# Kernel tuning notes

Measured on AMD Instinct MI355X. Metric: run time of the kernel, lower is better.

## Reference

```python
import jax, jax.numpy as jnp
import numpy as np

INPUT_SIZE = 4
HIDDEN = 100
OUTPUT = 1
SEQ_LEN = 65536


def setup_inputs() -> dict:
    key = jax.random.key(0)
    ks = jax.random.split(key, 7)
    s = 0.1  # small init scale, mimics torch's uniform(-1/sqrt(H), 1/sqrt(H))
    return {
        "input_seq": jax.random.normal(ks[0], (SEQ_LEN, INPUT_SIZE), dtype=jnp.float32),
        "W_ih": jax.random.normal(ks[1], (4 * HIDDEN, INPUT_SIZE), dtype=jnp.float32) * s,
        "W_hh": jax.random.normal(ks[2], (4 * HIDDEN, HIDDEN), dtype=jnp.float32) * s,
        "b_ih": jax.random.normal(ks[3], (4 * HIDDEN,), dtype=jnp.float32) * s,
        "b_hh": jax.random.normal(ks[4], (4 * HIDDEN,), dtype=jnp.float32) * s,
        "W_lin": jax.random.normal(ks[5], (OUTPUT, HIDDEN), dtype=jnp.float32) * s,
        "b_lin": jax.random.normal(ks[6], (OUTPUT,), dtype=jnp.float32) * s,
    }


def reference(input_seq, W_ih, W_hh, b_ih, b_hh, W_lin, b_lin):
    # Precompute the input contribution to all gates in one GEMM: [S, 4H]
    x_gates = input_seq @ W_ih.T + (b_ih + b_hh)

    def step(carry, xg):
        h, c = carry  # each [H]
        gates = xg + h @ W_hh.T  # [4H]
        # torch gate order: i, f, g, o
        i = jax.nn.sigmoid(gates[:HIDDEN])
        f = jax.nn.sigmoid(gates[HIDDEN:2 * HIDDEN])
        g = jnp.tanh(gates[2 * HIDDEN:3 * HIDDEN])
        o = jax.nn.sigmoid(gates[3 * HIDDEN:])
        c_new = f * c + i * g
        h_new = o * jnp.tanh(c_new)
        return (h_new, c_new), None

    h0 = jnp.zeros((HIDDEN,), dtype=input_seq.dtype)
    c0 = jnp.zeros((HIDDEN,), dtype=input_seq.dtype)
    (h_last, _), _ = jax.lax.scan(step, (h0, c0), x_gates)

    # predictions[-1] == linear applied to the last hidden state; shape [OUTPUT]
    return h_last @ W_lin.T + b_lin
```

## Files before the change

### kernel.cpp

```cpp
#include <hip/hip_runtime.h>

#define HIDDEN  100
#define SEQLEN  65536
#define XTILE   256
#define NT      256

typedef float    f32x4 __attribute__((ext_vector_type(4)));
typedef _Float16 h16x2 __attribute__((ext_vector_type(2)));

#define DPP_XOR1 0xB1
#define DPP_XOR2 0x4E

#if defined(__has_builtin) && __has_builtin(__builtin_amdgcn_rcpf)
#define RCPF(x) __builtin_amdgcn_rcpf(x)
#else
#define RCPF(x) (1.0f / (x))
#endif

#define QSWAP(v, ctrl) __int_as_float(__builtin_amdgcn_mov_dpp(__float_as_int(v), (ctrl), 0xf, 0xf, true))

static __device__ __forceinline__ h16x2 as_h2(unsigned u) {
    union { unsigned u; h16x2 h; } cv; cv.u = u; return cv.h;
}
static __device__ __forceinline__ unsigned as_u32(h16x2 h) {
    union { h16x2 h; unsigned u; } cv; cv.h = h; return cv.u;
}

static __device__ __forceinline__ float dot2(h16x2 a, h16x2 b, float c) {
#if defined(__has_builtin) && __has_builtin(__builtin_amdgcn_fdot2)
    return __builtin_amdgcn_fdot2(a, b, c, false);
#else
    return __builtin_fmaf((float)a.y, (float)b.y, __builtin_fmaf((float)a.x, (float)b.x, c));
#endif
}

__global__ __launch_bounds__(NT) __attribute__((amdgpu_waves_per_eu(1, 1)))
void lstm_seq6(const float* __restrict__ x,
               const float* __restrict__ W_ih,
               const float* __restrict__ W_hh,
               const float* __restrict__ b_ih,
               const float* __restrict__ b_hh,
               const float* __restrict__ W_lin,
               const float* __restrict__ b_lin,
               float* __restrict__ out)
{
    __shared__ __align__(16) unsigned hbuf[2][64];
    __shared__ __align__(16) f32x4 xs[XTILE];
    __shared__ float red[112];

    const int tid = threadIdx.x;
    const int j   = tid >> 1;
    const int p   = tid & 1;
    const bool active = (j < HIDDEN);

    const int rA = p ? (200 + j) : j;
    const int rB = p ? (300 + j) : (100 + j);

    h16x2 wA[52], wB[52];
    f32x4 wihA = (f32x4)(0.f), wihB = (f32x4)(0.f);
    float biasA = 0.f, biasB = 0.f;
#pragma unroll
    for (int q = 0; q < 52; ++q) { wA[q] = (h16x2)(_Float16)0; wB[q] = (h16x2)(_Float16)0; }
    if (active) {
        const float* a = W_hh + rA * HIDDEN;
        const float* b = W_hh + rB * HIDDEN;
#pragma unroll
        for (int q = 0; q < 50; ++q) {
            h16x2 pa, pb;
            pa.x = (_Float16)a[2*q]; pa.y = (_Float16)a[2*q+1];
            pb.x = (_Float16)b[2*q]; pb.y = (_Float16)b[2*q+1];
            wA[q] = pa; wB[q] = pb;
        }
        wihA  = reinterpret_cast<const f32x4*>(W_ih)[rA];
        wihB  = reinterpret_cast<const f32x4*>(W_ih)[rB];
        biasA = b_ih[rA] + b_hh[rA];
        biasB = b_ih[rB] + b_hh[rB];
    }
    const float mA  = p ? 2.0f : 1.0f;
    const float mA1 = mA - 1.0f;
    float c = 0.f;

    if (tid < 64) { hbuf[0][tid] = 0u; hbuf[1][tid] = 0u; }
    __syncthreads();

    auto step = [&](const unsigned* hr, unsigned* hw, const f32x4 xv) {
        float accA0 = __builtin_fmaf(wihA.x, xv.x, biasA);
        float accA1 = wihA.y * xv.y;
        accA0 = __builtin_fmaf(wihA.z, xv.z, accA0);
        accA1 = __builtin_fmaf(wihA.w, xv.w, accA1);
        float accB0 = __builtin_fmaf(wihB.x, xv.x, biasB);
        float accB1 = wihB.y * xv.y;
        accB0 = __builtin_fmaf(wihB.z, xv.z, accB0);
        accB1 = __builtin_fmaf(wihB.w, xv.w, accB1);

        const uint4* h4 = reinterpret_cast<const uint4*>(hr);
#pragma unroll
        for (int q = 0; q < 13; ++q) {
            uint4 hv = h4[q];
            h16x2 h0 = as_h2(hv.x), h1 = as_h2(hv.y), h2 = as_h2(hv.z), h3 = as_h2(hv.w);
            accA0 = dot2(wA[4*q+0], h0, accA0);
            accA1 = dot2(wA[4*q+1], h1, accA1);
            accA0 = dot2(wA[4*q+2], h2, accA0);
            accA1 = dot2(wA[4*q+3], h3, accA1);
            accB0 = dot2(wB[4*q+0], h0, accB0);
            accB1 = dot2(wB[4*q+1], h1, accB1);
            accB0 = dot2(wB[4*q+2], h2, accB0);
            accB1 = dot2(wB[4*q+3], h3, accB1);
        }
        float sA = accA0 + accA1;
        float sB = accB0 + accB1;

        float uA   = sA * mA;
        float actA = __builtin_fmaf(mA, RCPF(1.0f + __expf(-uA)), -mA1);
        float actB = RCPF(1.0f + __expf(-sB));

        float gA = QSWAP(actA, DPP_XOR1);
        float gB = QSWAP(actB, DPP_XOR1);

        float hval = 0.f;
        if (p == 0) {
            c = __builtin_fmaf(actB, c, actA * gA);
            float th = __builtin_fmaf(-2.0f, RCPF(1.0f + __expf(2.0f * c)), 1.0f);
            hval = gB * th;
        }
        float hpart = QSWAP(hval, DPP_XOR2);
        if ((tid & 3) == 0 && active) {
            h16x2 hp;
            hp.x = (_Float16)hval;
            hp.y = (_Float16)hpart;
            hw[tid >> 2] = as_u32(hp);
        }
        __syncthreads();
    };

    const f32x4* x4 = reinterpret_cast<const f32x4*>(x);
    for (int t0 = 0; t0 < SEQLEN; t0 += XTILE) {
        xs[tid] = x4[t0 + tid];
        __syncthreads();
        for (int tt = 0; tt < XTILE; tt += 2) {
            step(hbuf[0], hbuf[1], xs[tt]);
            step(hbuf[1], hbuf[0], xs[tt + 1]);
        }
    }

    if (tid < HIDDEN) {
        h16x2 hp = as_h2(hbuf[0][tid >> 1]);
        float hj = (tid & 1) ? (float)hp.y : (float)hp.x;
        red[tid] = hj * W_lin[tid];
    }
    __syncthreads();
    if (tid == 0) {
        float s = b_lin[0];
        for (int q = 0; q < HIDDEN; ++q) s += red[q];
        out[0] = s;
    }
}

extern "C" void kernel_launch(void* const* d_in, const int* in_sizes, int n_in,
                              void* d_out, int out_size, void* d_ws, size_t ws_size,
                              hipStream_t stream) {
    const float* x     = (const float*)d_in[0];
    const float* W_ih  = (const float*)d_in[1];
    const float* W_hh  = (const float*)d_in[2];
    const float* b_ih  = (const float*)d_in[3];
    const float* b_hh  = (const float*)d_in[4];
    const float* W_lin = (const float*)d_in[5];
    const float* b_lin = (const float*)d_in[6];
    float* out = (float*)d_out;

    lstm_seq6<<<dim3(1), dim3(NT), 0, stream>>>(
        x, W_ih, W_hh, b_ih, b_hh, W_lin, b_lin, out);
}
```

Baseline: 28.19 ms.

## Split hidden-dim reduction across thread pairs, each computing all four gates

Each pair of threads now splits the 100-wide hidden dot product in half (K-split) and computes partial sums for all four gates, combining them with a DPP swap. Both threads then evaluate all gate activations and the cell update redundantly, which removes the gate-exchange shuffles and the divergent p==0 branch. The h buffer is laid out in two padded halves so each thread reads only its 7 uint4 chunks, and h is packed with the cvt_pkrtz builtin when available, which rounds toward zero where the old casts used round-to-nearest. The cost is four extra reductions per step and redundant transcendental work on both threads of each pair.

```diff
diff --git a/kernel.cpp b/kernel.cpp
--- a/kernel.cpp
+++ b/kernel.cpp
@@ -22,10 +22,17 @@
 static __device__ __forceinline__ h16x2 as_h2(unsigned u) {
     union { unsigned u; h16x2 h; } cv; cv.u = u; return cv.h;
 }
-static __device__ __forceinline__ unsigned as_u32(h16x2 h) {
-    union { h16x2 h; unsigned u; } cv; cv.h = h; return cv.u;
+static __device__ __forceinline__ unsigned pack_f16(float a, float b) {
+#if defined(__has_builtin) && __has_builtin(__builtin_amdgcn_cvt_pkrtz)
+    auto v = __builtin_amdgcn_cvt_pkrtz(a, b);
+    union { decltype(v) h; unsigned u; } cv; cv.h = v;
+    return cv.u;
+#else
+    union { h16x2 h; unsigned u; } cv;
+    cv.h.x = (_Float16)a; cv.h.y = (_Float16)b;
+    return cv.u;
+#endif
 }
-
 static __device__ __forceinline__ float dot2(h16x2 a, h16x2 b, float c) {
 #if defined(__has_builtin) && __has_builtin(__builtin_amdgcn_fdot2)
     return __builtin_amdgcn_fdot2(a, b, c, false);
@@ -35,7 +42,7 @@
 }
 
 __global__ __launch_bounds__(NT) __attribute__((amdgpu_waves_per_eu(1, 1)))
-void lstm_seq6(const float* __restrict__ x,
+void lstm_seq7(const float* __restrict__ x,
                const float* __restrict__ W_ih,
                const float* __restrict__ W_hh,
                const float* __restrict__ b_ih,
@@ -52,83 +59,75 @@
     const int j   = tid >> 1;
     const int p   = tid & 1;
     const bool active = (j < HIDDEN);
+    const int jj  = active ? j : 0;
+    const int off = p * 50;
 
-    const int rA = p ? (200 + j) : j;
-    const int rB = p ? (300 + j) : (100 + j);
-
-    h16x2 wA[52], wB[52];
-    f32x4 wihA = (f32x4)(0.f), wihB = (f32x4)(0.f);
-    float biasA = 0.f, biasB = 0.f;
+    h16x2 w[4][28];
+    float wx0[4], wx1[4], bz[4];
 #pragma unroll
-    for (int q = 0; q < 52; ++q) { wA[q] = (h16x2)(_Float16)0; wB[q] = (h16x2)(_Float16)0; }
-    if (active) {
-        const float* a = W_hh + rA * HIDDEN;
-        const float* b = W_hh + rB * HIDDEN;
+    for (int g = 0; g < 4; ++g) {
+        const int row = g * HIDDEN + jj;
+        const float* wr = W_hh + row * HIDDEN + off;
 #pragma unroll
-        for (int q = 0; q < 50; ++q) {
-            h16x2 pa, pb;
-            pa.x = (_Float16)a[2*q]; pa.y = (_Float16)a[2*q+1];
-            pb.x = (_Float16)b[2*q]; pb.y = (_Float16)b[2*q+1];
-            wA[q] = pa; wB[q] = pb;
+        for (int q = 0; q < 25; ++q) {
+            h16x2 pw; pw.x = (_Float16)wr[2*q]; pw.y = (_Float16)wr[2*q+1];
+            w[g][q] = pw;
         }
-        wihA  = reinterpret_cast<const f32x4*>(W_ih)[rA];
-        wihB  = reinterpret_cast<const f32x4*>(W_ih)[rB];
-        biasA = b_ih[rA] + b_hh[rA];
-        biasB = b_ih[rB] + b_hh[rB];
+#pragma unroll
+        for (int q = 25; q < 28; ++q) w[g][q] = (h16x2)(_Float16)0;
+        const f32x4 wih = reinterpret_cast<const f32x4*>(W_ih)[row];
+        wx0[g] = p ? wih.z : wih.x;
+        wx1[g] = p ? wih.w : wih.y;
+        bz[g]  = p ? 0.f : (b_ih[row] + b_hh[row]);
     }
-    const float mA  = p ? 2.0f : 1.0f;
-    const float mA1 = mA - 1.0f;
     float c = 0.f;
 
     if (tid < 64) { hbuf[0][tid] = 0u; hbuf[1][tid] = 0u; }
     __syncthreads();
 
     auto step = [&](const unsigned* hr, unsigned* hw, const f32x4 xv) {
-        float accA0 = __builtin_fmaf(wihA.x, xv.x, biasA);
-        float accA1 = wihA.y * xv.y;
-        accA0 = __builtin_fmaf(wihA.z, xv.z, accA0);
-        accA1 = __builtin_fmaf(wihA.w, xv.w, accA1);
-        float accB0 = __builtin_fmaf(wihB.x, xv.x, biasB);
-        float accB1 = wihB.y * xv.y;
-        accB0 = __builtin_fmaf(wihB.z, xv.z, accB0);
-        accB1 = __builtin_fmaf(wihB.w, xv.w, accB1);
+        const uint4* h4 = reinterpret_cast<const uint4*>(hr + (p ? 28 : 0));
+        uint4 hv[7];
+#pragma unroll
+        for (int t = 0; t < 7; ++t) hv[t] = h4[t];
 
-        const uint4* h4 = reinterpret_cast<const uint4*>(hr);
+        const float xe0 = p ? xv.z : xv.x;
+        const float xe1 = p ? xv.w : xv.y;
+        float a0 = __builtin_fmaf(wx1[0], xe1, __builtin_fmaf(wx0[0], xe0, bz[0]));
+        float a1 = __builtin_fmaf(wx1[1], xe1, __builtin_fmaf(wx0[1], xe0, bz[1]));
+        float a2 = __builtin_fmaf(wx1[2], xe1, __builtin_fmaf(wx0[2], xe0, bz[2]));
+        float a3 = __builtin_fmaf(wx1[3], xe1, __builtin_fmaf(wx0[3], xe0, bz[3]));
 #pragma unroll
-        for (int q = 0; q < 13; ++q) {
-            uint4 hv = h4[q];
-            h16x2 h0 = as_h2(hv.x), h1 = as_h2(hv.y), h2 = as_h2(hv.z), h3 = as_h2(hv.w);
-            accA0 = dot2(wA[4*q+0], h0, accA0);
-            accA1 = dot2(wA[4*q+1], h1, accA1);
-            accA0 = dot2(wA[4*q+2], h2, accA0);
-            accA1 = dot2(wA[4*q+3], h3, accA1);
-            accB0 = dot2(wB[4*q+0], h0, accB0);
-            accB1 = dot2(wB[4*q+1], h1, accB1);
-            accB0 = dot2(wB[4*q+2], h2, accB0);
-            accB1 = dot2(wB[4*q+3], h3, accB1);
+        for (int t = 0; t < 7; ++t) {
+            const h16x2 h0 = as_h2(hv[t].x), h1 = as_h2(hv[t].y);
+            const h16x2 h2 = as_h2(hv[t].z), h3 = as_h2(hv[t].w);
+            a0 = dot2(w[0][4*t+0], h0, a0); a1 = dot2(w[1][4*t+0], h0, a1);
+            a2 = dot2(w[2][4*t+0], h0, a2); a3 = dot2(w[3][4*t+0], h0, a3);
+            a0 = dot2(w[0][4*t+1], h1, a0); a1 = dot2(w[1][4*t+1], h1, a1);
+            a2 = dot2(w[2][4*t+1], h1, a2); a3 = dot2(w[3][4*t+1], h1, a3);
+            a0 = dot2(w[0][4*t+2], h2, a0); a1 = dot2(w[1][4*t+2], h2, a1);
+            a2 = dot2(w[2][4*t+2], h2, a2); a3 = dot2(w[3][4*t+2], h2, a3);
+            a0 = dot2(w[0][4*t+3], h3, a0); a1 = dot2(w[1][4*t+3], h3, a1);
+            a2 = dot2(w[2][4*t+3], h3, a2); a3 = dot2(w[3][4*t+3], h3, a3);
         }
-        float sA = accA0 + accA1;
-        float sB = accB0 + accB1;
+        a0 += QSWAP(a0, DPP_XOR1);
+        a1 += QSWAP(a1, DPP_XOR1);
+        a2 += QSWAP(a2, DPP_XOR1);
+        a3 += QSWAP(a3, DPP_XOR1);
 
-        float uA   = sA * mA;
-        float actA = __builtin_fmaf(mA, RCPF(1.0f + __expf(-uA)), -mA1);
-        float actB = RCPF(1.0f + __expf(-sB));
+        const float i_ = RCPF(1.0f + __expf(-a0));
+        const float f_ = RCPF(1.0f + __expf(-a1));
+        const float g_ = __builtin_fmaf(-2.0f, RCPF(1.0f + __expf(2.0f * a2)), 1.0f);
+        const float o_ = RCPF(1.0f + __expf(-a3));
+        c = __builtin_fmaf(f_, c, i_ * g_);
+        const float th   = __builtin_fmaf(-2.0f, RCPF(1.0f + __expf(2.0f * c)), 1.0f);
+        const float hval = o_ * th;
 
-        float gA = QSWAP(actA, DPP_XOR1);
-        float gB = QSWAP(actB, DPP_XOR1);
-
-        float hval = 0.f;
-        if (p == 0) {
-            c = __builtin_fmaf(actB, c, actA * gA);
-            float th = __builtin_fmaf(-2.0f, RCPF(1.0f + __expf(2.0f * c)), 1.0f);
-            hval = gB * th;
-        }
-        float hpart = QSWAP(hval, DPP_XOR2);
+        const float hoth = QSWAP(hval, DPP_XOR2);
         if ((tid & 3) == 0 && active) {
-            h16x2 hp;
-            hp.x = (_Float16)hval;
-            hp.y = (_Float16)hpart;
-            hw[tid >> 2] = as_u32(hp);
+            const int m  = tid >> 2;
+            const int dw = (m < 25) ? m : m + 3;
+            hw[dw] = pack_f16(hval, hoth);
         }
         __syncthreads();
     };
@@ -144,8 +143,9 @@
     }
 
     if (tid < HIDDEN) {
-        h16x2 hp = as_h2(hbuf[0][tid >> 1]);
-        float hj = (tid & 1) ? (float)hp.y : (float)hp.x;
+        const int slot = (tid < 50) ? tid : tid + 6;
+        const h16x2 hp = as_h2(hbuf[0][slot >> 1]);
+        const float hj = (slot & 1) ? (float)hp.y : (float)hp.x;
         red[tid] = hj * W_lin[tid];
     }
     __syncthreads();
@@ -168,6 +168,6 @@
     const float* b_lin = (const float*)d_in[6];
     float* out = (float*)d_out;
 
-    lstm_seq6<<<dim3(1), dim3(NT), 0, stream>>>(
+    lstm_seq7<<<dim3(1), dim3(NT), 0, stream>>>(
         x, W_ih, W_hh, b_ih, b_hh, W_lin, b_lin, out);
 }
```

Result: faster. 26.69 ms (-5.3%).
